# Kernel optimization log

Hardware: AMD Instinct MI355X
Metric: run time of the kernel (lower is better)

Reference implementation:

```python
import jax, jax.numpy as jnp
import numpy as np

H = 768  # bert-base hidden size; match MLP width = 2*H = 1536


def setup_inputs() -> dict:
    key = jax.random.key(0)
    ks = jax.random.split(key, 6)
    B, S = 2, 256
    std = 0.02  # TruncatedNormal(stddev=initializer_range)
    return {
        "hidden": jax.random.normal(ks[0], (B, S, H), dtype=jnp.float32),
        "w_start": jax.random.normal(ks[1], (H, 1), dtype=jnp.float32) * std,
        "b_start": jnp.zeros((1,), jnp.float32),
        "w_end": jax.random.normal(ks[2], (H, 1), dtype=jnp.float32) * std,
        "b_end": jnp.zeros((1,), jnp.float32),
        "w1": jax.random.normal(ks[3], (2 * H, 2 * H), dtype=jnp.float32) * std,
        "b1": jnp.zeros((2 * H,), jnp.float32),
        "w2": jax.random.normal(ks[4], (2 * H, 1), dtype=jnp.float32) * std,
        "b2": jnp.zeros((1,), jnp.float32),
    }


def reference(hidden, w_start, b_start, w_end, b_end, w1, b1, w2, b2):
    # hidden: [B, S, H] = BERT sequence output (dropout disabled at inference)
    start_logits = hidden @ w_start + b_start  # [B, S, 1]
    end_logits = hidden @ w_end + b_end        # [B, S, 1]

    # Pairwise span features: concat(row_i, col_j) along last dim, fed to dense1.
    # concat([row, col]) @ w1 == row @ w1[:H] + col @ w1[H:], so we split w1 and
    # broadcast-add instead of materializing the [B,S,S,2H] concat tile.
    row_proj = hidden @ w1[:H]   # [B, S, 2H] (start-token contribution)
    col_proj = hidden @ w1[H:]   # [B, S, 2H] (end-token contribution)
    pre = row_proj[:, :, None, :] + col_proj[:, None, :, :] + b1  # [B, S, S, 2H]
    act = jax.nn.gelu(pre, approximate=False)  # keras 'gelu' is exact
    match_logits = act @ w2 + b2  # [B, S, S, 1]
    return start_logits, end_logits, match_logits
```

## Files before the change

kernel.cpp:

```cpp
#include <hip/hip_runtime.h>
#include <stdint.h>

typedef __attribute__((ext_vector_type(8))) __bf16 bf16x8;
typedef __attribute__((ext_vector_type(4))) float  floatx4;
typedef __attribute__((ext_vector_type(4))) unsigned int uint4v;
typedef __attribute__((ext_vector_type(2))) unsigned int uint2v;
typedef __attribute__((ext_vector_type(4))) float  float4v;
typedef __attribute__((ext_vector_type(2))) _Float16 half2v;
typedef unsigned int u32;

__device__ __forceinline__ unsigned short f2bf(float f) {
  union { float f; unsigned int u; } x; x.f = f;
  unsigned int r = x.u + 0x7fffu + ((x.u >> 16) & 1u);
  return (unsigned short)(r >> 16);
}

__global__ __launch_bounds__(256) void convert_kernel(
    const float* __restrict__ hidden, const float* __restrict__ w1,
    unsigned short* __restrict__ wsH, unsigned short* __restrict__ wsW1) {
  int t = blockIdx.x * 256 + threadIdx.x;
  const float* src; unsigned short* dst; int idx;
  if (t < 49152) { src = hidden; dst = wsH; idx = t * 8; }
  else           { src = w1;     dst = wsW1; idx = (t - 49152) * 8; }
  float4v v0 = *(const float4v*)(src + idx);
  float4v v1 = *(const float4v*)(src + idx + 4);
  uint4v o;
  o[0] = (u32)f2bf(v0[0]) | ((u32)f2bf(v0[1]) << 16);
  o[1] = (u32)f2bf(v0[2]) | ((u32)f2bf(v0[3]) << 16);
  o[2] = (u32)f2bf(v1[0]) | ((u32)f2bf(v1[1]) << 16);
  o[3] = (u32)f2bf(v1[2]) | ((u32)f2bf(v1[3]) << 16);
  *(uint4v*)(dst + idx) = o;
}

__global__ __launch_bounds__(256) void proj_kernel(
    const unsigned short* __restrict__ wsH, const unsigned short* __restrict__ wsW1,
    const float* __restrict__ hidden,
    const float* __restrict__ b1, unsigned short* __restrict__ wsR,
    unsigned short* __restrict__ wsC,
    const float* __restrict__ w_start, const float* __restrict__ b_start,
    const float* __restrict__ w_end, const float* __restrict__ b_end,
    const float* __restrict__ b2, float* __restrict__ out) {
  const int tid  = threadIdx.x;
  if (blockIdx.y == 16) {
    if (blockIdx.x >= 32) {
      float v = b2[0];
      float4v vv = {v, v, v, v};
      int base = (blockIdx.x - 32) * 8192 + tid * 4;
#pragma unroll
      for (int itr = 0; itr < 8; ++itr)
        *(float4v*)(out + 1024 + base + itr * 1024) = vv;
      return;
    }
    const int lane = tid & 63;
    const int wv   = tid >> 6;
    const int wg   = blockIdx.x * 4 + wv;
    float wsv[12], wev[12];
#pragma unroll
    for (int t = 0; t < 12; ++t) {
      wsv[t] = w_start[lane + 64 * t];
      wev[t] = w_end[lane + 64 * t];
    }
    const float bs = b_start[0];
    const float be = b_end[0];
#pragma unroll
    for (int r = 0; r < 4; ++r) {
      int row = wg * 4 + r;
      const float* h = hidden + (size_t)row * 768;
      float ps = 0.f, pe = 0.f;
#pragma unroll
      for (int t = 0; t < 12; ++t) {
        float hv = h[lane + 64 * t];
        ps += hv * wsv[t];
        pe += hv * wev[t];
      }
#pragma unroll
      for (int off = 32; off >= 1; off >>= 1) {
        ps += __shfl_xor(ps, off, 64);
        pe += __shfl_xor(pe, off, 64);
      }
      if (lane == 0) { out[row] = ps + bs; out[512 + row] = pe + be; }
    }
    return;
  }

  __shared__ short As[4 * 32 * 8];
  __shared__ short Bs[4 * 64 * 8];

  const int lane = tid & 63;
  const int wave = tid >> 6;
  const int wr = wave >> 1, wc = wave & 1;
  const int m0 = blockIdx.y * 32;
  const int n0g = blockIdx.x * 64;
  const bool isR = (n0g < 1536);
  const int kbase = isR ? 0 : 768;
  const int n0 = isR ? n0g : (n0g - 1536);
  const int q = lane >> 4, l15 = lane & 15;

  floatx4 acc0 = {}, acc1 = {};

  const int a_row = tid >> 3;
  const int a_s   = tid & 7;
  const int b_n   = tid & 63;
  const int b_kg  = tid >> 6;

  const unsigned short* hrow = wsH + (size_t)(m0 + a_row) * 768 + a_s * 4;
  const unsigned short* bcol = wsW1 + (size_t)(kbase + b_kg * 8) * 1536 + n0 + b_n;

  uint2v au = *(const uint2v*)(hrow);
  unsigned short bv[8];
#pragma unroll
  for (int a = 0; a < 8; ++a) bv[a] = bcol[(size_t)a * 1536];

  const int aq = a_s >> 1;
  const int aj = (a_s & 1) * 4;

  for (int ko = 0; ko < 768; ko += 32) {
    *(uint2v*)(&As[(aq * 32 + a_row) * 8 + aj]) = au;
    uint4v pv;
#pragma unroll
    for (int a = 0; a < 4; ++a)
      pv[a] = (u32)bv[2 * a] | ((u32)bv[2 * a + 1] << 16);
    *(uint4v*)(&Bs[(b_kg * 64 + b_n) * 8]) = pv;
    __syncthreads();

    if (ko + 32 < 768) {
      au = *(const uint2v*)(hrow + ko + 32);
      const unsigned short* bp = bcol + (size_t)(ko + 32) * 1536;
#pragma unroll
      for (int a = 0; a < 8; ++a) bv[a] = bp[(size_t)a * 1536];
    }

    bf16x8 af  = *(const bf16x8*)(&As[(q * 32 + 16 * wr + l15) * 8]);
    bf16x8 bg0 = *(const bf16x8*)(&Bs[(q * 64 + 32 * wc + l15) * 8]);
    bf16x8 bg1 = *(const bf16x8*)(&Bs[(q * 64 + 32 * wc + 16 + l15) * 8]);
    acc0 = __builtin_amdgcn_mfma_f32_16x16x32_bf16(af, bg0, acc0, 0, 0, 0);
    acc1 = __builtin_amdgcn_mfma_f32_16x16x32_bf16(af, bg1, acc1, 0, 0, 0);
    __syncthreads();
  }

  unsigned short* outp = isR ? wsR : wsC;
#pragma unroll
  for (int ni = 0; ni < 2; ++ni) {
    const floatx4& ac = ni ? acc1 : acc0;
    int col = n0 + 32 * wc + 16 * ni + l15;
    float bias = isR ? b1[col] : 0.0f;
#pragma unroll
    for (int r = 0; r < 4; ++r) {
      int rowg = m0 + 16 * wr + q * 4 + r;
      outp[(size_t)rowg * 1536 + col] = f2bf(ac[r] + bias);
    }
  }
}

__device__ __forceinline__ u32 ph_add(u32 a, u32 b) {
  u32 d; asm("v_pk_add_f16 %0, %1, %2" : "=v"(d) : "v"(a), "v"(b)); return d;
}
__device__ __forceinline__ u32 ph_mul(u32 a, u32 b) {
  u32 d; asm("v_pk_mul_f16 %0, %1, %2" : "=v"(d) : "v"(a), "v"(b)); return d;
}
__device__ __forceinline__ u32 ph_fma(u32 a, u32 b, u32 c) {
  u32 d; asm("v_pk_fma_f16 %0, %1, %2, %3" : "=v"(d) : "v"(a), "v"(b), "v"(c)); return d;
}
__device__ __forceinline__ u32 ph_max(u32 a, u32 b) {
  u32 d; asm("v_pk_max_f16 %0, %1, %2" : "=v"(d) : "v"(a), "v"(b)); return d;
}
__device__ __forceinline__ u32 ph_min(u32 a, u32 b) {
  u32 d; asm("v_pk_min_f16 %0, %1, %2" : "=v"(d) : "v"(a), "v"(b)); return d;
}
__device__ __forceinline__ u32 h2c(float f) {
  _Float16 h = (_Float16)f;
  unsigned short s = __builtin_bit_cast(unsigned short, h);
  return (u32)s | ((u32)s << 16);
}

__device__ __forceinline__ void gelu_pair(float& acc, u32 r, u32 c, u32 w,
                                          u32 C0c, u32 C1c, u32 C2c, u32 C3c,
                                          u32 LOc, u32 HIc, u32 Hc) {
  u32 x  = ph_add(r, c);
  u32 xc = ph_min(ph_max(x, LOc), HIc);
  u32 u  = ph_mul(xc, xc);
  u32 p  = ph_fma(u, ph_fma(u, ph_fma(u, C3c, C2c), C1c), C0c);
  u32 t  = ph_fma(xc, p, Hc);
  u32 g  = ph_mul(x, t);
  acc = __builtin_amdgcn_fdot2(__builtin_bit_cast(half2v, g),
                               __builtin_bit_cast(half2v, w), acc, false);
}

__device__ __forceinline__ uint4v bf8_to_h8(uint4v v) {
  uint4v o;
#pragma unroll
  for (int a = 0; a < 4; ++a) {
    union { unsigned int u; float f; } lo, hi;
    lo.u = v[a] << 16;
    hi.u = v[a] & 0xffff0000u;
    auto h = __builtin_amdgcn_cvt_pkrtz(lo.f, hi.f);
    o[a] = __builtin_bit_cast(unsigned int, h);
  }
  return o;
}

__global__ __launch_bounds__(256) void match_kernel(
    const unsigned short* __restrict__ wsR,
    const unsigned short* __restrict__ wsC,
    const float* __restrict__ w2,
    float* __restrict__ outm) {
  __shared__ unsigned int RsU[32 * 68];
  __shared__ unsigned int CsU[64 * 68];
  __shared__ unsigned int WsU[64];

  const int tid = threadIdx.x;
  const int jt = blockIdx.x;
  const int it = blockIdx.y;
  const int bz = blockIdx.z / 12;
  const int kh = blockIdx.z % 12;
  const int Kb = kh * 128;

  const int rg  = tid >> 4;
  const int cgl = tid & 15;

  const u32 C0c = h2c(0.39103831f);
  const u32 C1c = h2c(-0.05415410f);
  const u32 C2c = h2c(0.00461682f);
  const u32 C3c = h2c(-1.51033e-4f);
  const u32 LOc = h2c(-3.5f);
  const u32 HIc = h2c(3.5f);
  const u32 Hc  = h2c(0.5f);

  float accA0 = 0.f, accA1 = 0.f, accA2 = 0.f, accA3 = 0.f;
  float accB0 = 0.f, accB1 = 0.f, accB2 = 0.f, accB3 = 0.f;

  const int srow = tid >> 3;
  const int sseg = tid & 7;
#pragma unroll
  for (int ps = 0; ps < 2; ++ps) {
    const unsigned short* g =
        wsR + (size_t)(bz * 256 + it * 32 + srow) * 1536 + Kb + ps * 64 + sseg * 8;
    *(uint4v*)(RsU + srow * 68 + ps * 32 + sseg * 4) = bf8_to_h8(*(const uint4v*)g);
  }
#pragma unroll
  for (int a = 0; a < 2; ++a) {
    int row = srow + 32 * a;
#pragma unroll
    for (int ps = 0; ps < 2; ++ps) {
      const unsigned short* g =
          wsC + (size_t)(bz * 256 + jt * 64 + row) * 1536 + Kb + ps * 64 + sseg * 8;
      *(uint4v*)(CsU + row * 68 + ps * 32 + sseg * 4) = bf8_to_h8(*(const uint4v*)g);
    }
  }
  if (tid < 64) {
    auto h = __builtin_amdgcn_cvt_pkrtz(w2[Kb + 2 * tid], w2[Kb + 2 * tid + 1]);
    WsU[tid] = __builtin_bit_cast(unsigned int, h);
  }
  __syncthreads();

  const unsigned int* rap = RsU + (2 * rg + 0) * 68;
  const unsigned int* rbp = RsU + (2 * rg + 1) * 68;
  const unsigned int* c0p = CsU + (cgl +  0) * 68;
  const unsigned int* c1p = CsU + (cgl + 16) * 68;
  const unsigned int* c2p = CsU + (cgl + 32) * 68;
  const unsigned int* c3p = CsU + (cgl + 48) * 68;

#pragma unroll 2
  for (int ks = 0; ks < 16; ++ks) {
    uint4v ra = *(const uint4v*)(rap + ks * 4);
    uint4v rb = *(const uint4v*)(rbp + ks * 4);
    uint4v wv = *(const uint4v*)(WsU + ks * 4);
    {
      uint4v cv = *(const uint4v*)(c0p + ks * 4);
#pragma unroll
      for (int p = 0; p < 4; ++p) {
        gelu_pair(accA0, ra[p], cv[p], wv[p], C0c, C1c, C2c, C3c, LOc, HIc, Hc);
        gelu_pair(accB0, rb[p], cv[p], wv[p], C0c, C1c, C2c, C3c, LOc, HIc, Hc);
      }
    }
    {
      uint4v cv = *(const uint4v*)(c1p + ks * 4);
#pragma unroll
      for (int p = 0; p < 4; ++p) {
        gelu_pair(accA1, ra[p], cv[p], wv[p], C0c, C1c, C2c, C3c, LOc, HIc, Hc);
        gelu_pair(accB1, rb[p], cv[p], wv[p], C0c, C1c, C2c, C3c, LOc, HIc, Hc);
      }
    }
    {
      uint4v cv = *(const uint4v*)(c2p + ks * 4);
#pragma unroll
      for (int p = 0; p < 4; ++p) {
        gelu_pair(accA2, ra[p], cv[p], wv[p], C0c, C1c, C2c, C3c, LOc, HIc, Hc);
        gelu_pair(accB2, rb[p], cv[p], wv[p], C0c, C1c, C2c, C3c, LOc, HIc, Hc);
      }
    }
    {
      uint4v cv = *(const uint4v*)(c3p + ks * 4);
#pragma unroll
      for (int p = 0; p < 4; ++p) {
        gelu_pair(accA3, ra[p], cv[p], wv[p], C0c, C1c, C2c, C3c, LOc, HIc, Hc);
        gelu_pair(accB3, rb[p], cv[p], wv[p], C0c, C1c, C2c, C3c, LOc, HIc, Hc);
      }
    }
  }

  const size_t rowA = (size_t)(bz * 256 + it * 32 + 2 * rg);
  const size_t base = rowA * 256 + jt * 64 + cgl;
  unsafeAtomicAdd(&outm[base +  0], accA0);
  unsafeAtomicAdd(&outm[base + 16], accA1);
  unsafeAtomicAdd(&outm[base + 32], accA2);
  unsafeAtomicAdd(&outm[base + 48], accA3);
  unsafeAtomicAdd(&outm[base + 256 +  0], accB0);
  unsafeAtomicAdd(&outm[base + 256 + 16], accB1);
  unsafeAtomicAdd(&outm[base + 256 + 32], accB2);
  unsafeAtomicAdd(&outm[base + 256 + 48], accB3);
}

extern "C" void kernel_launch(void* const* d_in, const int* in_sizes, int n_in,
                              void* d_out, int out_size, void* d_ws, size_t ws_size,
                              hipStream_t stream) {
  const float* hidden  = (const float*)d_in[0];
  const float* w_start = (const float*)d_in[1];
  const float* b_start = (const float*)d_in[2];
  const float* w_end   = (const float*)d_in[3];
  const float* b_end   = (const float*)d_in[4];
  const float* w1      = (const float*)d_in[5];
  const float* b1      = (const float*)d_in[6];
  const float* w2      = (const float*)d_in[7];
  const float* b2      = (const float*)d_in[8];

  float* out = (float*)d_out;
  char* ws = (char*)d_ws;
  unsigned short* wsR  = (unsigned short*)(ws);
  unsigned short* wsC  = (unsigned short*)(ws + 1572864);
  unsigned short* wsH  = (unsigned short*)(ws + 3145728);
  unsigned short* wsW1 = (unsigned short*)(ws + 3932160);

  convert_kernel<<<dim3(1344), dim3(256), 0, stream>>>(hidden, w1, wsH, wsW1);
  proj_kernel<<<dim3(48, 17), dim3(256), 0, stream>>>(
      wsH, wsW1, hidden, b1, wsR, wsC, w_start, b_start, w_end, b_end, b2, out);
  match_kernel<<<dim3(4, 8, 24), dim3(256), 0, stream>>>(wsR, wsC, w2, out + 1024);
}
```

Before: 129.0 us.

## Fuse bf16 conversion into projection GEMM and double-buffer match kernel K-loop

Drops the separate fp32-to-bf16 convert kernel and converts hidden/w1 values in registers while staging tiles in the projection GEMM. This removes one launch and a workspace round trip. The match kernel moves to 512-thread blocks that each loop over three 128-wide K chunks with double-buffered shared memory, overlapping global loads with GELU compute, so it uses fewer blocks and issues fewer atomics. In exchange the GEMM reads twice the bytes (fp32) per tile, the match grid shrinks to 256 blocks, and per-block shared memory doubles.

```diff
diff --git a/kernel.cpp b/kernel.cpp
--- a/kernel.cpp
+++ b/kernel.cpp
@@ -15,26 +15,8 @@
   return (unsigned short)(r >> 16);
 }
 
-__global__ __launch_bounds__(256) void convert_kernel(
+__global__ __launch_bounds__(256) void proj_kernel(
     const float* __restrict__ hidden, const float* __restrict__ w1,
-    unsigned short* __restrict__ wsH, unsigned short* __restrict__ wsW1) {
-  int t = blockIdx.x * 256 + threadIdx.x;
-  const float* src; unsigned short* dst; int idx;
-  if (t < 49152) { src = hidden; dst = wsH; idx = t * 8; }
-  else           { src = w1;     dst = wsW1; idx = (t - 49152) * 8; }
-  float4v v0 = *(const float4v*)(src + idx);
-  float4v v1 = *(const float4v*)(src + idx + 4);
-  uint4v o;
-  o[0] = (u32)f2bf(v0[0]) | ((u32)f2bf(v0[1]) << 16);
-  o[1] = (u32)f2bf(v0[2]) | ((u32)f2bf(v0[3]) << 16);
-  o[2] = (u32)f2bf(v1[0]) | ((u32)f2bf(v1[1]) << 16);
-  o[3] = (u32)f2bf(v1[2]) | ((u32)f2bf(v1[3]) << 16);
-  *(uint4v*)(dst + idx) = o;
-}
-
-__global__ __launch_bounds__(256) void proj_kernel(
-    const unsigned short* __restrict__ wsH, const unsigned short* __restrict__ wsW1,
-    const float* __restrict__ hidden,
     const float* __restrict__ b1, unsigned short* __restrict__ wsR,
     unsigned short* __restrict__ wsC,
     const float* __restrict__ w_start, const float* __restrict__ b_start,
@@ -103,11 +85,11 @@
   const int b_n   = tid & 63;
   const int b_kg  = tid >> 6;
 
-  const unsigned short* hrow = wsH + (size_t)(m0 + a_row) * 768 + a_s * 4;
-  const unsigned short* bcol = wsW1 + (size_t)(kbase + b_kg * 8) * 1536 + n0 + b_n;
-
-  uint2v au = *(const uint2v*)(hrow);
-  unsigned short bv[8];
+  const float* hrow = hidden + (size_t)(m0 + a_row) * 768 + a_s * 4;
+  const float* bcol = w1 + (size_t)(kbase + b_kg * 8) * 1536 + n0 + b_n;
+
+  float4v hv = *(const float4v*)(hrow);
+  float bv[8];
 #pragma unroll
   for (int a = 0; a < 8; ++a) bv[a] = bcol[(size_t)a * 1536];
 
@@ -115,17 +97,23 @@
   const int aj = (a_s & 1) * 4;
 
   for (int ko = 0; ko < 768; ko += 32) {
+    uint2v au;
+    au[0] = (u32)f2bf(hv[0]) | ((u32)f2bf(hv[1]) << 16);
+    au[1] = (u32)f2bf(hv[2]) | ((u32)f2bf(hv[3]) << 16);
     *(uint2v*)(&As[(aq * 32 + a_row) * 8 + aj]) = au;
     uint4v pv;
 #pragma unroll
-    for (int a = 0; a < 4; ++a)
-      pv[a] = (u32)bv[2 * a] | ((u32)bv[2 * a + 1] << 16);
+    for (int a = 0; a < 4; ++a) {
+      u32 lo = f2bf(bv[2 * a]);
+      u32 hi = f2bf(bv[2 * a + 1]);
+      pv[a] = lo | (hi << 16);
+    }
     *(uint4v*)(&Bs[(b_kg * 64 + b_n) * 8]) = pv;
     __syncthreads();
 
     if (ko + 32 < 768) {
-      au = *(const uint2v*)(hrow + ko + 32);
-      const unsigned short* bp = bcol + (size_t)(ko + 32) * 1536;
+      hv = *(const float4v*)(hrow + ko + 32);
+      const float* bp = bcol + (size_t)(ko + 32) * 1536;
 #pragma unroll
       for (int a = 0; a < 8; ++a) bv[a] = bp[(size_t)a * 1536];
     }
@@ -199,24 +187,26 @@
   return o;
 }
 
-__global__ __launch_bounds__(256) void match_kernel(
+__global__ __launch_bounds__(512) void match_kernel(
     const unsigned short* __restrict__ wsR,
     const unsigned short* __restrict__ wsC,
     const float* __restrict__ w2,
     float* __restrict__ outm) {
-  __shared__ unsigned int RsU[32 * 68];
-  __shared__ unsigned int CsU[64 * 68];
-  __shared__ unsigned int WsU[64];
+  __shared__ u32 RsU[2][32 * 68];
+  __shared__ u32 CsU[2][64 * 68];
+  __shared__ u32 WsU[2][64];
 
   const int tid = threadIdx.x;
   const int jt = blockIdx.x;
   const int it = blockIdx.y;
-  const int bz = blockIdx.z / 12;
-  const int kh = blockIdx.z % 12;
-  const int Kb = kh * 128;
-
-  const int rg  = tid >> 4;
-  const int cgl = tid & 15;
+  const int bz = blockIdx.z >> 2;
+  const int kb4 = blockIdx.z & 3;
+  const int Kb0 = kb4 * 384;
+
+  const int rg  = tid >> 5;
+  const int cg  = tid & 31;
+  const int srow = tid >> 4;
+  const int sseg = tid & 15;
 
   const u32 C0c = h2c(0.39103831f);
   const u32 C1c = h2c(-0.05415410f);
@@ -226,89 +216,79 @@
   const u32 HIc = h2c(3.5f);
   const u32 Hc  = h2c(0.5f);
 
-  float accA0 = 0.f, accA1 = 0.f, accA2 = 0.f, accA3 = 0.f;
-  float accB0 = 0.f, accB1 = 0.f, accB2 = 0.f, accB3 = 0.f;
-
-  const int srow = tid >> 3;
-  const int sseg = tid & 7;
-#pragma unroll
-  for (int ps = 0; ps < 2; ++ps) {
-    const unsigned short* g =
-        wsR + (size_t)(bz * 256 + it * 32 + srow) * 1536 + Kb + ps * 64 + sseg * 8;
-    *(uint4v*)(RsU + srow * 68 + ps * 32 + sseg * 4) = bf8_to_h8(*(const uint4v*)g);
-  }
-#pragma unroll
-  for (int a = 0; a < 2; ++a) {
-    int row = srow + 32 * a;
-#pragma unroll
-    for (int ps = 0; ps < 2; ++ps) {
-      const unsigned short* g =
-          wsC + (size_t)(bz * 256 + jt * 64 + row) * 1536 + Kb + ps * 64 + sseg * 8;
-      *(uint4v*)(CsU + row * 68 + ps * 32 + sseg * 4) = bf8_to_h8(*(const uint4v*)g);
-    }
-  }
-  if (tid < 64) {
-    auto h = __builtin_amdgcn_cvt_pkrtz(w2[Kb + 2 * tid], w2[Kb + 2 * tid + 1]);
-    WsU[tid] = __builtin_bit_cast(unsigned int, h);
-  }
+  float a0 = 0.f, a1 = 0.f, b0 = 0.f, b1 = 0.f;
+
+  const unsigned short* gR  = wsR + (size_t)(bz * 256 + it * 32 + srow) * 1536 + sseg * 8;
+  const unsigned short* gC0 = wsC + (size_t)(bz * 256 + jt * 64 + srow) * 1536 + sseg * 8;
+  const unsigned short* gC1 = gC0 + (size_t)32 * 1536;
+
+  auto wr = [&](int buf, uint4v pR, uint4v pC0, uint4v pC1, float w0, float w1) {
+    *(uint4v*)(&RsU[buf][srow * 68 + sseg * 4]) = bf8_to_h8(pR);
+    *(uint4v*)(&CsU[buf][srow * 68 + sseg * 4]) = bf8_to_h8(pC0);
+    *(uint4v*)(&CsU[buf][(srow + 32) * 68 + sseg * 4]) = bf8_to_h8(pC1);
+    if (tid < 64) {
+      auto h = __builtin_amdgcn_cvt_pkrtz(w0, w1);
+      WsU[buf][tid] = __builtin_bit_cast(u32, h);
+    }
+  };
+  auto comp = [&](int buf) {
+    const u32* rap = &RsU[buf][(2 * rg) * 68];
+    const u32* rbp = rap + 68;
+    const u32* c0p = &CsU[buf][cg * 68];
+    const u32* c1p = c0p + 32 * 68;
+    const u32* wp  = &WsU[buf][0];
+#pragma unroll 4
+    for (int ks = 0; ks < 16; ++ks) {
+      uint4v ra = *(const uint4v*)(rap + ks * 4);
+      uint4v rb = *(const uint4v*)(rbp + ks * 4);
+      uint4v wv = *(const uint4v*)(wp + ks * 4);
+      uint4v cv = *(const uint4v*)(c0p + ks * 4);
+#pragma unroll
+      for (int p = 0; p < 4; ++p) {
+        gelu_pair(a0, ra[p], cv[p], wv[p], C0c, C1c, C2c, C3c, LOc, HIc, Hc);
+        gelu_pair(b0, rb[p], cv[p], wv[p], C0c, C1c, C2c, C3c, LOc, HIc, Hc);
+      }
+      uint4v cw = *(const uint4v*)(c1p + ks * 4);
+#pragma unroll
+      for (int p = 0; p < 4; ++p) {
+        gelu_pair(a1, ra[p], cw[p], wv[p], C0c, C1c, C2c, C3c, LOc, HIc, Hc);
+        gelu_pair(b1, rb[p], cw[p], wv[p], C0c, C1c, C2c, C3c, LOc, HIc, Hc);
+      }
+    }
+  };
+
+  uint4v pR  = *(const uint4v*)(gR + Kb0);
+  uint4v pC0 = *(const uint4v*)(gC0 + Kb0);
+  uint4v pC1 = *(const uint4v*)(gC1 + Kb0);
+  float pw0 = 0.f, pw1 = 0.f;
+  if (tid < 64) { pw0 = w2[Kb0 + 2 * tid]; pw1 = w2[Kb0 + 2 * tid + 1]; }
+  wr(0, pR, pC0, pC1, pw0, pw1);
   __syncthreads();
 
-  const unsigned int* rap = RsU + (2 * rg + 0) * 68;
-  const unsigned int* rbp = RsU + (2 * rg + 1) * 68;
-  const unsigned int* c0p = CsU + (cgl +  0) * 68;
-  const unsigned int* c1p = CsU + (cgl + 16) * 68;
-  const unsigned int* c2p = CsU + (cgl + 32) * 68;
-  const unsigned int* c3p = CsU + (cgl + 48) * 68;
-
-#pragma unroll 2
-  for (int ks = 0; ks < 16; ++ks) {
-    uint4v ra = *(const uint4v*)(rap + ks * 4);
-    uint4v rb = *(const uint4v*)(rbp + ks * 4);
-    uint4v wv = *(const uint4v*)(WsU + ks * 4);
-    {
-      uint4v cv = *(const uint4v*)(c0p + ks * 4);
-#pragma unroll
-      for (int p = 0; p < 4; ++p) {
-        gelu_pair(accA0, ra[p], cv[p], wv[p], C0c, C1c, C2c, C3c, LOc, HIc, Hc);
-        gelu_pair(accB0, rb[p], cv[p], wv[p], C0c, C1c, C2c, C3c, LOc, HIc, Hc);
-      }
-    }
-    {
-      uint4v cv = *(const uint4v*)(c1p + ks * 4);
-#pragma unroll
-      for (int p = 0; p < 4; ++p) {
-        gelu_pair(accA1, ra[p], cv[p], wv[p], C0c, C1c, C2c, C3c, LOc, HIc, Hc);
-        gelu_pair(accB1, rb[p], cv[p], wv[p], C0c, C1c, C2c, C3c, LOc, HIc, Hc);
-      }
-    }
-    {
-      uint4v cv = *(const uint4v*)(c2p + ks * 4);
-#pragma unroll
-      for (int p = 0; p < 4; ++p) {
-        gelu_pair(accA2, ra[p], cv[p], wv[p], C0c, C1c, C2c, C3c, LOc, HIc, Hc);
-        gelu_pair(accB2, rb[p], cv[p], wv[p], C0c, C1c, C2c, C3c, LOc, HIc, Hc);
-      }
-    }
-    {
-      uint4v cv = *(const uint4v*)(c3p + ks * 4);
-#pragma unroll
-      for (int p = 0; p < 4; ++p) {
-        gelu_pair(accA3, ra[p], cv[p], wv[p], C0c, C1c, C2c, C3c, LOc, HIc, Hc);
-        gelu_pair(accB3, rb[p], cv[p], wv[p], C0c, C1c, C2c, C3c, LOc, HIc, Hc);
-      }
-    }
-  }
+  pR  = *(const uint4v*)(gR + Kb0 + 128);
+  pC0 = *(const uint4v*)(gC0 + Kb0 + 128);
+  pC1 = *(const uint4v*)(gC1 + Kb0 + 128);
+  if (tid < 64) { pw0 = w2[Kb0 + 128 + 2 * tid]; pw1 = w2[Kb0 + 128 + 2 * tid + 1]; }
+  comp(0);
+  wr(1, pR, pC0, pC1, pw0, pw1);
+  __syncthreads();
+
+  pR  = *(const uint4v*)(gR + Kb0 + 256);
+  pC0 = *(const uint4v*)(gC0 + Kb0 + 256);
+  pC1 = *(const uint4v*)(gC1 + Kb0 + 256);
+  if (tid < 64) { pw0 = w2[Kb0 + 256 + 2 * tid]; pw1 = w2[Kb0 + 256 + 2 * tid + 1]; }
+  comp(1);
+  wr(0, pR, pC0, pC1, pw0, pw1);
+  __syncthreads();
+
+  comp(0);
 
   const size_t rowA = (size_t)(bz * 256 + it * 32 + 2 * rg);
-  const size_t base = rowA * 256 + jt * 64 + cgl;
-  unsafeAtomicAdd(&outm[base +  0], accA0);
-  unsafeAtomicAdd(&outm[base + 16], accA1);
-  unsafeAtomicAdd(&outm[base + 32], accA2);
-  unsafeAtomicAdd(&outm[base + 48], accA3);
-  unsafeAtomicAdd(&outm[base + 256 +  0], accB0);
-  unsafeAtomicAdd(&outm[base + 256 + 16], accB1);
-  unsafeAtomicAdd(&outm[base + 256 + 32], accB2);
-  unsafeAtomicAdd(&outm[base + 256 + 48], accB3);
+  const size_t base = rowA * 256 + jt * 64 + cg;
+  unsafeAtomicAdd(&outm[base +  0], a0);
+  unsafeAtomicAdd(&outm[base + 32], a1);
+  unsafeAtomicAdd(&outm[base + 256 +  0], b0);
+  unsafeAtomicAdd(&outm[base + 256 + 32], b1);
 }
 
 extern "C" void kernel_launch(void* const* d_in, const int* in_sizes, int n_in,
@@ -326,13 +306,10 @@
 
   float* out = (float*)d_out;
   char* ws = (char*)d_ws;
-  unsigned short* wsR  = (unsigned short*)(ws);
-  unsigned short* wsC  = (unsigned short*)(ws + 1572864);
-  unsigned short* wsH  = (unsigned short*)(ws + 3145728);
-  unsigned short* wsW1 = (unsigned short*)(ws + 3932160);
-
-  convert_kernel<<<dim3(1344), dim3(256), 0, stream>>>(hidden, w1, wsH, wsW1);
+  unsigned short* wsR = (unsigned short*)(ws);
+  unsigned short* wsC = (unsigned short*)(ws + 1572864);
+
   proj_kernel<<<dim3(48, 17), dim3(256), 0, stream>>>(
-      wsH, wsW1, hidden, b1, wsR, wsC, w_start, b_start, w_end, b_end, b2, out);
-  match_kernel<<<dim3(4, 8, 24), dim3(256), 0, stream>>>(wsR, wsC, w2, out + 1024);
-}
+      hidden, w1, b1, wsR, wsC, w_start, b_start, w_end, b_end, b2, out);
+  match_kernel<<<dim3(4, 8, 8), dim3(512), 0, stream>>>(wsR, wsC, w2, out + 1024);
+}
```

New measurement: 126.2 us. 2.1% less time.
